# Kernel optimization log

Measured on AMD Instinct MI355X. Metric: run time of the kernel, lower is better.

Reference implementation:

```python
import jax, jax.numpy as jnp
import numpy as np

B, S, I, H, O = 256, 2048, 32, 128, 1


def setup_inputs() -> dict:
    key = jax.random.key(0)
    ks = jax.random.split(key, 9)
    sI = 1.0 / np.sqrt(I)
    sH = 1.0 / np.sqrt(H)
    sD = 1.0 / np.sqrt(H * S)
    return {
        "x": jax.random.normal(ks[0], (B, S, I), jnp.float32),
        "Wi": jax.random.normal(ks[1], (I, H), jnp.float32) * sI,
        "bi": jax.random.normal(ks[2], (H,), jnp.float32) * sI,
        "Wh": jax.random.normal(ks[3], (H, H), jnp.float32) * sH,
        "bh": jax.random.normal(ks[4], (H,), jnp.float32) * sH,
        "Wa": jax.random.normal(ks[5], (H, 1), jnp.float32) * sH,
        "ba": jax.random.normal(ks[6], (1,), jnp.float32) * sH,
        "Wd": jax.random.normal(ks[7], (H * S, O), jnp.float32) * sD,
        "bd": jax.random.normal(ks[8], (O,), jnp.float32) * sD,
        "resDepth": 4,
    }


def _branch_ids(seq_len: int, resDepth: int) -> np.ndarray:
    # Encodes the per-step branch of ResRNN_Cell.forward (static in i, resDepth):
    # 0: i==0 (set hstart, h0 stays zero)   1: i==lag-2 -> h0=tanh(hn+hstart)
    # 4: resDepth==1 -> h0=tanh(hn+h0)      2: i%resDepth==0 -> h0=tanh(hn+ht), ht=hn
    # 3: else -> h0=tanh(hn)
    br = np.full(seq_len, 3, dtype=np.int32)
    br[(np.arange(seq_len) % resDepth) == 0] = 2
    if resDepth == 1:
        br[:] = 4
    br[seq_len - 2] = 1
    br[0] = 0
    return br


def reference(x, Wi, bi, Wh, bh, Wa, ba, Wd, bd, resDepth):
    batch, seq_len, _ = x.shape
    hid = Wh.shape[0]
    br = _branch_ids(seq_len, int(resDepth))
    f0, f1, f2, f4 = (jnp.asarray(br == k) for k in (0, 1, 2, 4))
    xs = jnp.swapaxes(x, 0, 1)  # (S, B, I)
    z = jnp.zeros((batch, hid), x.dtype)

    def step(carry, inp):
        h0, ht, hstart = carry
        xt, g0, g1, g2, g4 = inp
        hn = xt @ Wi + bi + h0 @ Wh + bh  # (B, H)
        hstart = jnp.where(g0, hn, hstart)
        cand = jnp.where(g1, jnp.tanh(hn + hstart),
               jnp.where(g4, jnp.tanh(hn + h0),
               jnp.where(g2, jnp.tanh(hn + ht), jnp.tanh(hn))))
        h0n = jnp.where(g0, h0, cand)  # at i==0 h0 is NOT updated in the original
        htn = jnp.where(g2, hn, ht)
        return (h0n, htn, hstart), hn

    _, hiddens = jax.lax.scan(step, (z, z, z), (xs, f0, f1, f2, f4))
    # hiddens: (S, B, H) == torch.cat(outputs, 0)
    scores = hiddens @ Wa + ba  # (S, B, 1)
    # faithful to the original's .view((batchSize, -1)) on (S,B,1)-contiguous data
    att = jax.nn.softmax(scores.reshape(batch, seq_len), axis=-1)
    att = att.reshape(seq_len, batch, 1)
    weighted = hiddens * att  # (S, B, H)
    # faithful to .view(-1, hiddenNum * seq_len) on (S,B,H)-contiguous data
    flat = weighted.reshape(batch, seq_len * hid)
    return flat @ Wd + bd
```

## Files before the change

### kernel.cpp

```cpp
#include <hip/hip_runtime.h>
#include <math.h>

#define B_ 256
#define S_ 2048
#define I_ 32
#define H_ 128

typedef float v2f __attribute__((ext_vector_type(2)));
__device__ __forceinline__ v2f mk2(float a, float b) { v2f r; r.x = a; r.y = b; return r; }

__device__ __forceinline__ void pk_fma(v2f& d, v2f a, v2f b) {
    asm("v_pk_fma_f32 %0, %1, %2, %0" : "+v"(d) : "v"(a), "v"(b));
}
__device__ __forceinline__ void pk_fma_lo(v2f& d, v2f a, v2f b) {
    asm("v_pk_fma_f32 %0, %1, %2, %0 op_sel:[0,0,0] op_sel_hi:[0,1,1]"
        : "+v"(d) : "v"(a), "v"(b));
}
__device__ __forceinline__ void pk_fma_hi(v2f& d, v2f a, v2f b) {
    asm("v_pk_fma_f32 %0, %1, %2, %0 op_sel:[1,0,0] op_sel_hi:[1,1,1]"
        : "+v"(d) : "v"(a), "v"(b));
}

__device__ __forceinline__ void sync_lds() {
    asm volatile("" ::: "memory");
    asm volatile("s_waitcnt lgkmcnt(0)" ::: "memory");
    __builtin_amdgcn_s_barrier();
    asm volatile("" ::: "memory");
}

__device__ __forceinline__ float fast_tanh(float z) {
    float e = __expf(2.0f * z);
    return 1.0f - 2.0f / (e + 1.0f);
}

template <int CTRL>
__device__ __forceinline__ float dppf(float v) {
    return __int_as_float(__builtin_amdgcn_update_dpp(
        0, __float_as_int(v), CTRL, 0xF, 0xF, false));
}

__device__ __forceinline__ float swz_xor16(float v) {
    return __int_as_float(__builtin_amdgcn_ds_swizzle(__float_as_int(v), 0x401F));
}

#define PKQ(hv, q)                                                \
    pk_fma_lo(accA, mk2((hv).x, (hv).y), WhP[4 * (q) + 0]);       \
    pk_fma_hi(accA, mk2((hv).x, (hv).y), WhP[4 * (q) + 1]);       \
    pk_fma_lo(accB, mk2((hv).z, (hv).w), WhP[4 * (q) + 2]);       \
    pk_fma_hi(accB, mk2((hv).z, (hv).w), WhP[4 * (q) + 3]);

#define UP_REDUCE(RING)                                                       \
    {                                                                         \
      float r = uP;                                                           \
      r += dppf<0xB1>(r);                                                     \
      r += dppf<0x124>(r);                                                    \
      if ((l & 0xD) == 0)                                                     \
        ((float*)&pl_lds[RING][(w << 2) | ((l >> 4) & 3)])[(l >> 1) & 1] = r; \
    }

#define PL_COMBINE(RING, SIDX)                                                \
    {                                                                         \
      float2 pp = pl_lds[RING][l & 31];                                       \
      float px = pp.x, py = pp.y;                                             \
      px += dppf<0xB1>(px);  py += dppf<0xB1>(py);                            \
      px += dppf<0x4E>(px);  py += dppf<0x4E>(py);                            \
      px += dppf<0x141>(px); py += dppf<0x141>(py);                           \
      px += dppf<0x128>(px); py += dppf<0x128>(py);                           \
      px += swz_xor16(px);   py += swz_xor16(py);                             \
      if (l == 0) part[((SIDX) << 8) + b] = make_float2(px, py);              \
    }

#define MAT_CORE(XA, XB)                                                      \
    v2f xw01 = mk2(biasR, 0.0f);                                              \
    pk_fma(xw01, mk2((XA).x, (XA).y), WiP[0]);                                \
    pk_fma(xw01, mk2((XA).z, (XA).w), WiP[1]);                                \
    pk_fma(xw01, mk2((XB).x, (XB).y), WiP[2]);                                \
    pk_fma(xw01, mk2((XB).z, (XB).w), WiP[3]);                                \
    v2f accA = mk2(0.0f, 0.0f), accB = mk2(0.0f, 0.0f);                       \
    PKQ(hv0, 0) PKQ(hv1, 1) PKQ(hv2, 2) PKQ(hv3, 3)                           \
    float a0 = accA.x + accB.x;                                               \
    float a1 = accA.y + accB.y;                                               \
    a0 += dppf<0xB1>(a0);                                                     \
    a1 += dppf<0xB1>(a1);                                                     \
    float tt = kb0b ? a1 : a0;                                                \
    tt += xw01.x + xw01.y;                                                    \
    tt += dppf<0x4E>(tt);                                                     \
    tt += dppf<0x128>(tt);                                                    \
    const float hn = tt;

#define STEP_FULL(g, PH, XA, XB, CPH)                                         \
  {                                                                           \
    const int s_ = (g) * 8 + (PH);                                            \
    const float4* hsrc = (const float4*)&h0_lds[(PH) & 1][0];                 \
    float4 hv0 = hsrc[kg];                                                    \
    float4 hv1 = hsrc[kg + 8];                                                \
    float4 hv2 = hsrc[kg + 16];                                               \
    float4 hv3 = hsrc[kg + 24];                                               \
    if (s_ >= 1) UP_REDUCE(((PH) + 3) & 3)                                    \
    if (w == (PH) && s_ >= 2) PL_COMBINE(((PH) + 2) & 3, s_ - 2)              \
    MAT_CORE(XA, XB)                                                          \
    if (s_ < S_ - 2) {                                                        \
      const float4* xr = (const float4*)(xgrp + ((PH) + 2) * I_);             \
      (XA) = xr[0]; (XB) = xr[1];                                             \
    }                                                                         \
    uP = hn * (CPH);                                                          \
    float h0n;                                                                \
    if (s_ == 0)            { hstartR = hn; h0n = 0.0f; }                     \
    else if (s_ == S_ - 2)  { h0n = fast_tanh(hn + hstartR); }                \
    else if (rd == 1)       { h0n = fast_tanh(hn + h0R); }                    \
    else if (cnt == 0)      { h0n = fast_tanh(hn + htR); htR = hn; }          \
    else                    { h0n = fast_tanh(hn); }                          \
    h0R = h0n;                                                                \
    if (wmask) h0_lds[((PH) + 1) & 1][hf] = h0n;                              \
    cnt = (cnt + 1 == rd) ? 0 : cnt + 1;                                      \
    sync_lds();                                                               \
  }

#define STEP_LEAN4(g, PH, XA, XB, CPH)                                        \
  {                                                                           \
    const float4* hsrc = (const float4*)&h0_lds[(PH) & 1][0];                 \
    float4 hv0 = hsrc[kg];                                                    \
    float4 hv1 = hsrc[kg + 8];                                                \
    float4 hv2 = hsrc[kg + 16];                                               \
    float4 hv3 = hsrc[kg + 24];                                               \
    UP_REDUCE(((PH) + 3) & 3)                                                 \
    if (w == (PH)) PL_COMBINE(((PH) + 2) & 3, (g) * 8 + (PH) - 2)             \
    MAT_CORE(XA, XB)                                                          \
    {                                                                         \
      const float4* xr = (const float4*)(xgrp + ((PH) + 2) * I_);             \
      (XA) = xr[0]; (XB) = xr[1];                                             \
    }                                                                         \
    uP = hn * (CPH);                                                          \
    float h0n;                                                                \
    if (((PH) & 3) == 0) { h0n = fast_tanh(hn + htR); htR = hn; }             \
    else                 { h0n = fast_tanh(hn); }                             \
    if (wmask) h0_lds[((PH) + 1) & 1][hf] = h0n;                              \
    sync_lds();                                                               \
  }

#define STEP_LEAN(g, PH, XA, XB, CPH)                                         \
  {                                                                           \
    const float4* hsrc = (const float4*)&h0_lds[(PH) & 1][0];                 \
    float4 hv0 = hsrc[kg];                                                    \
    float4 hv1 = hsrc[kg + 8];                                                \
    float4 hv2 = hsrc[kg + 16];                                               \
    float4 hv3 = hsrc[kg + 24];                                               \
    UP_REDUCE(((PH) + 3) & 3)                                                 \
    if (w == (PH)) PL_COMBINE(((PH) + 2) & 3, (g) * 8 + (PH) - 2)             \
    MAT_CORE(XA, XB)                                                          \
    {                                                                         \
      const float4* xr = (const float4*)(xgrp + ((PH) + 2) * I_);             \
      (XA) = xr[0]; (XB) = xr[1];                                             \
    }                                                                         \
    uP = hn * (CPH);                                                          \
    const bool c0 = (cnt == 0);                                               \
    float resid = rd1 ? h0R : (c0 ? htR : 0.0f);                              \
    float h0n = fast_tanh(hn + resid);                                        \
    htR = (htup && c0) ? hn : htR;                                            \
    h0R = h0n;                                                                \
    if (wmask) h0_lds[((PH) + 1) & 1][hf] = h0n;                              \
    cnt = (cnt + 1 == rd) ? 0 : cnt + 1;                                      \
    sync_lds();                                                               \
  }

__global__ __launch_bounds__(512)
__attribute__((amdgpu_waves_per_eu(2, 2)))
void rnn_kernel(
    const float* __restrict__ x, const float* __restrict__ Wi,
    const float* __restrict__ bi, const float* __restrict__ Wh,
    const float* __restrict__ bh, const float* __restrict__ Wa,
    const float* __restrict__ Wd, const int* __restrict__ rdp,
    float2* __restrict__ part)
{
    const int b = blockIdx.x;
    const int t = threadIdx.x;
    const int w = t >> 6;
    const int l = t & 63;
    const int  kg    = (l & 3) | (((l >> 3) & 1) << 2);
    const int  hg    = ((l >> 2) & 1) | (((l >> 4) & 1) << 1)
                     | (((l >> 5) & 1) << 2);
    const int  hbase = 16 * w + 2 * hg;
    const int  hf    = hbase + (l & 1);
    const bool kb0b  = (l & 1);
    const bool wmask = ((l & 0xA) == 0);
    const int  i0x   = 8 * (((l >> 1) & 1) | (((l >> 3) & 1) << 1));

    __shared__ __align__(16) float h0_lds[2][H_];
    __shared__ __align__(8)  float2 pl_lds[4][32];

    const int rd = rdp[0];
    const bool rd1  = (rd == 1);
    const bool htup = !rd1;
    if (t < H_) h0_lds[0][t] = 0.0f;

    v2f WhP[16];
#pragma unroll
    for (int j = 0; j < 4; ++j)
#pragma unroll
        for (int c = 0; c < 4; ++c) {
            int k = 4 * kg + 32 * j + c;
            float2 wv = *(const float2*)(Wh + (size_t)k * H_ + hbase);
            WhP[4 * j + c] = mk2(wv.x, wv.y);
        }
    v2f WiP[4];
#pragma unroll
    for (int j = 0; j < 4; ++j) {
        float w0 = Wi[(size_t)(i0x + 2 * j) * H_ + hf];
        float w1 = Wi[(size_t)(i0x + 2 * j + 1) * H_ + hf];
        WiP[j] = mk2(w0, w1);
    }
    const float biasR = wmask ? (bi[hf] + bh[hf]) : 0.0f;

    const bool clsq = (l >> 1) & 1;
    const float waC = Wa[hf];
    float cph[8];
#pragma unroll
    for (int K = 0; K < 8; ++K)
        cph[K] = clsq ? Wd[(K << 15) + (b << 7) + hf] : waC;

    const float* xgrp = x + (size_t)b * (S_ * I_) + i0x;
    float4 xA0 = ((const float4*)xgrp)[0];
    float4 xB0 = ((const float4*)xgrp)[1];
    float4 xA1 = ((const float4*)(xgrp + I_))[0];
    float4 xB1 = ((const float4*)(xgrp + I_))[1];

    sync_lds();

    float htR = 0.f, hstartR = 0.f, h0R = 0.f;
    float uP = 0.f;
    int cnt = 0;

    {
        STEP_FULL(0, 0, xA0, xB0, cph[0])
        STEP_FULL(0, 1, xA1, xB1, cph[1])
        STEP_FULL(0, 2, xA0, xB0, cph[2])
        STEP_FULL(0, 3, xA1, xB1, cph[3])
        STEP_FULL(0, 4, xA0, xB0, cph[4])
        STEP_FULL(0, 5, xA1, xB1, cph[5])
        STEP_FULL(0, 6, xA0, xB0, cph[6])
        STEP_FULL(0, 7, xA1, xB1, cph[7])
        xgrp += 8 * I_;
    }
    if (rd == 4) {
        for (int g = 1; g < 255; ++g) {
            STEP_LEAN4(g, 0, xA0, xB0, cph[0])
            STEP_LEAN4(g, 1, xA1, xB1, cph[1])
            STEP_LEAN4(g, 2, xA0, xB0, cph[2])
            STEP_LEAN4(g, 3, xA1, xB1, cph[3])
            STEP_LEAN4(g, 4, xA0, xB0, cph[4])
            STEP_LEAN4(g, 5, xA1, xB1, cph[5])
            STEP_LEAN4(g, 6, xA0, xB0, cph[6])
            STEP_LEAN4(g, 7, xA1, xB1, cph[7])
            xgrp += 8 * I_;
        }
        cnt = 0;
    } else {
        for (int g = 1; g < 255; ++g) {
            STEP_LEAN(g, 0, xA0, xB0, cph[0])
            STEP_LEAN(g, 1, xA1, xB1, cph[1])
            STEP_LEAN(g, 2, xA0, xB0, cph[2])
            STEP_LEAN(g, 3, xA1, xB1, cph[3])
            STEP_LEAN(g, 4, xA0, xB0, cph[4])
            STEP_LEAN(g, 5, xA1, xB1, cph[5])
            STEP_LEAN(g, 6, xA0, xB0, cph[6])
            STEP_LEAN(g, 7, xA1, xB1, cph[7])
            xgrp += 8 * I_;
        }
    }
    {
        STEP_FULL(255, 0, xA0, xB0, cph[0])
        STEP_FULL(255, 1, xA1, xB1, cph[1])
        STEP_FULL(255, 2, xA0, xB0, cph[2])
        STEP_FULL(255, 3, xA1, xB1, cph[3])
        STEP_FULL(255, 4, xA0, xB0, cph[4])
        STEP_FULL(255, 5, xA1, xB1, cph[5])
        STEP_FULL(255, 6, xA0, xB0, cph[6])
        STEP_FULL(255, 7, xA1, xB1, cph[7])
    }

    UP_REDUCE(3)
    sync_lds();
    if (w == 0) PL_COMBINE(2, S_ - 2)
    if (w == 1) PL_COMBINE(3, S_ - 1)
}

__global__ __launch_bounds__(256) void attn_kernel(
    const float2* __restrict__ part, const float* __restrict__ bd,
    float* __restrict__ out)
{
    const int r = blockIdx.x;
    const int t = threadIdx.x;
    float sc[8], dv[8];
    float mx = -1e30f;
#pragma unroll
    for (int u = 0; u < 8; ++u) {
        int f = (r << 11) + (u << 8) + t;
        float2 a = part[f];
        sc[u] = a.x;
        dv[u] = a.y;
        mx = fmaxf(mx, sc[u]);
    }
    __shared__ float redm[4], redz[4], redw[4];
#pragma unroll
    for (int off = 32; off > 0; off >>= 1) mx = fmaxf(mx, __shfl_xor(mx, off, 64));
    if ((t & 63) == 0) redm[t >> 6] = mx;
    __syncthreads();
    mx = fmaxf(fmaxf(redm[0], redm[1]), fmaxf(redm[2], redm[3]));
    float z = 0.f, wv = 0.f;
#pragma unroll
    for (int u = 0; u < 8; ++u) {
        float e = __expf(sc[u] - mx);
        z += e;
        wv += e * dv[u];
    }
#pragma unroll
    for (int off = 32; off > 0; off >>= 1) {
        z += __shfl_xor(z, off, 64);
        wv += __shfl_xor(wv, off, 64);
    }
    if ((t & 63) == 0) { redz[t >> 6] = z; redw[t >> 6] = wv; }
    __syncthreads();
    if (t == 0) {
        float Z = redz[0] + redz[1] + redz[2] + redz[3];
        float W = redw[0] + redw[1] + redw[2] + redw[3];
        out[r] = bd[0] + W / Z;
    }
}

extern "C" void kernel_launch(void* const* d_in, const int* in_sizes, int n_in,
                              void* d_out, int out_size, void* d_ws, size_t ws_size,
                              hipStream_t stream) {
    const float* x  = (const float*)d_in[0];
    const float* Wi = (const float*)d_in[1];
    const float* bi = (const float*)d_in[2];
    const float* Wh = (const float*)d_in[3];
    const float* bh = (const float*)d_in[4];
    const float* Wa = (const float*)d_in[5];
    const float* Wd = (const float*)d_in[7];
    const float* bd = (const float*)d_in[8];
    const int*  rdp = (const int*)d_in[9];

    float2* part = (float2*)d_ws;

    rnn_kernel<<<B_, 512, 0, stream>>>(x, Wi, bi, Wh, bh, Wa, Wd, rdp, part);
    attn_kernel<<<B_, 256, 0, stream>>>(part, bd, (float*)d_out);
}
```

Measured before the change: 863.4 us.

## Remap recurrent matvec to 4 outputs x 8 k per lane with padded LDS

After: 863.1 us. About the same (-0.0%).

```diff
diff --git a/kernel.cpp b/kernel.cpp
--- a/kernel.cpp
+++ b/kernel.cpp
@@ -9,9 +9,6 @@
 typedef float v2f __attribute__((ext_vector_type(2)));
 __device__ __forceinline__ v2f mk2(float a, float b) { v2f r; r.x = a; r.y = b; return r; }
 
-__device__ __forceinline__ void pk_fma(v2f& d, v2f a, v2f b) {
-    asm("v_pk_fma_f32 %0, %1, %2, %0" : "+v"(d) : "v"(a), "v"(b));
-}
 __device__ __forceinline__ void pk_fma_lo(v2f& d, v2f a, v2f b) {
     asm("v_pk_fma_f32 %0, %1, %2, %0 op_sel:[0,0,0] op_sel_hi:[0,1,1]"
         : "+v"(d) : "v"(a), "v"(b));
@@ -43,19 +40,25 @@
     return __int_as_float(__builtin_amdgcn_ds_swizzle(__float_as_int(v), 0x401F));
 }
 
-#define PKQ(hv, q)                                                \
-    pk_fma_lo(accA, mk2((hv).x, (hv).y), WhP[4 * (q) + 0]);       \
-    pk_fma_hi(accA, mk2((hv).x, (hv).y), WhP[4 * (q) + 1]);       \
-    pk_fma_lo(accB, mk2((hv).z, (hv).w), WhP[4 * (q) + 2]);       \
-    pk_fma_hi(accB, mk2((hv).z, (hv).w), WhP[4 * (q) + 3]);
+#define CHP 12
+
+#define PKD(hv, base)                                             \
+    pk_fma_lo(acc01, mk2((hv).x, (hv).y), W01[(base) + 0]);       \
+    pk_fma_lo(acc23, mk2((hv).x, (hv).y), W23[(base) + 0]);       \
+    pk_fma_hi(acc01, mk2((hv).x, (hv).y), W01[(base) + 1]);       \
+    pk_fma_hi(acc23, mk2((hv).x, (hv).y), W23[(base) + 1]);       \
+    pk_fma_lo(acc01, mk2((hv).z, (hv).w), W01[(base) + 2]);       \
+    pk_fma_lo(acc23, mk2((hv).z, (hv).w), W23[(base) + 2]);       \
+    pk_fma_hi(acc01, mk2((hv).z, (hv).w), W01[(base) + 3]);       \
+    pk_fma_hi(acc23, mk2((hv).z, (hv).w), W23[(base) + 3]);
 
 #define UP_REDUCE(RING)                                                       \
     {                                                                         \
       float r = uP;                                                           \
       r += dppf<0xB1>(r);                                                     \
-      r += dppf<0x124>(r);                                                    \
-      if ((l & 0xD) == 0)                                                     \
-        ((float*)&pl_lds[RING][(w << 2) | ((l >> 4) & 3)])[(l >> 1) & 1] = r; \
+      r += dppf<0x4E>(r);                                                     \
+      if ((l & 0xB) == 0)                                                     \
+        ((float*)&pl_lds[RING][(w << 2) | ((l >> 4) & 3)])[(l >> 2) & 1] = r; \
     }
 
 #define PL_COMBINE(RING, SIDX)                                                \
@@ -70,38 +73,40 @@
       if (l == 0) part[((SIDX) << 8) + b] = make_float2(px, py);              \
     }
 
-#define MAT_CORE(XA, XB)                                                      \
-    v2f xw01 = mk2(biasR, 0.0f);                                              \
-    pk_fma(xw01, mk2((XA).x, (XA).y), WiP[0]);                                \
-    pk_fma(xw01, mk2((XA).z, (XA).w), WiP[1]);                                \
-    pk_fma(xw01, mk2((XB).x, (XB).y), WiP[2]);                                \
-    pk_fma(xw01, mk2((XB).z, (XB).w), WiP[3]);                                \
-    v2f accA = mk2(0.0f, 0.0f), accB = mk2(0.0f, 0.0f);                       \
-    PKQ(hv0, 0) PKQ(hv1, 1) PKQ(hv2, 2) PKQ(hv3, 3)                           \
-    float a0 = accA.x + accB.x;                                               \
-    float a1 = accA.y + accB.y;                                               \
-    a0 += dppf<0xB1>(a0);                                                     \
-    a1 += dppf<0xB1>(a1);                                                     \
-    float tt = kb0b ? a1 : a0;                                                \
-    tt += xw01.x + xw01.y;                                                    \
-    tt += dppf<0x4E>(tt);                                                     \
+#define MAT_CORE(XS)                                                          \
+    v2f acc01 = bias01, acc23 = bias23;                                       \
+    pk_fma_lo(acc01, mk2((XS).x, (XS).y), WiF01[0]);                          \
+    pk_fma_hi(acc01, mk2((XS).x, (XS).y), WiF01[1]);                          \
+    pk_fma_lo(acc23, mk2((XS).x, (XS).y), WiF23[0]);                          \
+    pk_fma_hi(acc23, mk2((XS).x, (XS).y), WiF23[1]);                          \
+    PKD(hvA, 0) PKD(hvB, 4)                                                   \
+    float p0 = acc01.x + dppf<0x141>(acc01.x);                                \
+    float p1 = acc01.y + dppf<0x141>(acc01.y);                                \
+    float p2 = acc23.x + dppf<0x141>(acc23.x);                                \
+    float p3 = acc23.y + dppf<0x141>(acc23.y);                                \
+    float s01x = p0 + dppf<0xB1>(p0);                                         \
+    float s01y = p1 + dppf<0xB1>(p1);                                         \
+    float s23x = p2 + dppf<0xB1>(p2);                                         \
+    float s23y = p3 + dppf<0xB1>(p3);                                         \
+    float t0 = kb0 ? s01y : s01x;                                             \
+    float t1 = kb0 ? s23y : s23x;                                             \
+    t0 += dppf<0x4E>(t0);                                                     \
+    t1 += dppf<0x4E>(t1);                                                     \
+    float tt = kb1 ? t1 : t0;                                                 \
     tt += dppf<0x128>(tt);                                                    \
     const float hn = tt;
 
-#define STEP_FULL(g, PH, XA, XB, CPH)                                         \
+#define STEP_FULL(g, PH, XS, CPH)                                             \
   {                                                                           \
     const int s_ = (g) * 8 + (PH);                                            \
-    const float4* hsrc = (const float4*)&h0_lds[(PH) & 1][0];                 \
-    float4 hv0 = hsrc[kg];                                                    \
-    float4 hv1 = hsrc[kg + 8];                                                \
-    float4 hv2 = hsrc[kg + 16];                                               \
-    float4 hv3 = hsrc[kg + 24];                                               \
+    const float* hb = &h0_lds[(PH) & 1][0];                                   \
+    float4 hvA = *(const float4*)(hb + rdoff);                                \
+    float4 hvB = *(const float4*)(hb + rdoff + 4);                            \
     if (s_ >= 1) UP_REDUCE(((PH) + 3) & 3)                                    \
     if (w == (PH) && s_ >= 2) PL_COMBINE(((PH) + 2) & 3, s_ - 2)              \
-    MAT_CORE(XA, XB)                                                          \
+    MAT_CORE(XS)                                                              \
     if (s_ < S_ - 2) {                                                        \
-      const float4* xr = (const float4*)(xgrp + ((PH) + 2) * I_);             \
-      (XA) = xr[0]; (XB) = xr[1];                                             \
+      (XS) = *(const float2*)(xgrp + ((PH) + 2) * I_);                        \
     }                                                                         \
     uP = hn * (CPH);                                                          \
     float h0n;                                                                \
@@ -111,54 +116,44 @@
     else if (cnt == 0)      { h0n = fast_tanh(hn + htR); htR = hn; }          \
     else                    { h0n = fast_tanh(hn); }                          \
     h0R = h0n;                                                                \
-    if (wmask) h0_lds[((PH) + 1) & 1][hf] = h0n;                              \
+    if (wmask) h0_lds[((PH) + 1) & 1][hwoff] = h0n;                           \
     cnt = (cnt + 1 == rd) ? 0 : cnt + 1;                                      \
     sync_lds();                                                               \
   }
 
-#define STEP_LEAN4(g, PH, XA, XB, CPH)                                        \
+#define STEP_LEAN4(g, PH, XS, CPH)                                            \
   {                                                                           \
-    const float4* hsrc = (const float4*)&h0_lds[(PH) & 1][0];                 \
-    float4 hv0 = hsrc[kg];                                                    \
-    float4 hv1 = hsrc[kg + 8];                                                \
-    float4 hv2 = hsrc[kg + 16];                                               \
-    float4 hv3 = hsrc[kg + 24];                                               \
+    const float* hb = &h0_lds[(PH) & 1][0];                                   \
+    float4 hvA = *(const float4*)(hb + rdoff);                                \
+    float4 hvB = *(const float4*)(hb + rdoff + 4);                            \
     UP_REDUCE(((PH) + 3) & 3)                                                 \
     if (w == (PH)) PL_COMBINE(((PH) + 2) & 3, (g) * 8 + (PH) - 2)             \
-    MAT_CORE(XA, XB)                                                          \
-    {                                                                         \
-      const float4* xr = (const float4*)(xgrp + ((PH) + 2) * I_);             \
-      (XA) = xr[0]; (XB) = xr[1];                                             \
-    }                                                                         \
+    MAT_CORE(XS)                                                              \
+    (XS) = *(const float2*)(xgrp + ((PH) + 2) * I_);                          \
     uP = hn * (CPH);                                                          \
     float h0n;                                                                \
     if (((PH) & 3) == 0) { h0n = fast_tanh(hn + htR); htR = hn; }             \
     else                 { h0n = fast_tanh(hn); }                             \
-    if (wmask) h0_lds[((PH) + 1) & 1][hf] = h0n;                              \
+    if (wmask) h0_lds[((PH) + 1) & 1][hwoff] = h0n;                           \
     sync_lds();                                                               \
   }
 
-#define STEP_LEAN(g, PH, XA, XB, CPH)                                         \
+#define STEP_LEAN(g, PH, XS, CPH)                                             \
   {                                                                           \
-    const float4* hsrc = (const float4*)&h0_lds[(PH) & 1][0];                 \
-    float4 hv0 = hsrc[kg];                                                    \
-    float4 hv1 = hsrc[kg + 8];                                                \
-    float4 hv2 = hsrc[kg + 16];                                               \
-    float4 hv3 = hsrc[kg + 24];                                               \
+    const float* hb = &h0_lds[(PH) & 1][0];                                   \
+    float4 hvA = *(const float4*)(hb + rdoff);                                \
+    float4 hvB = *(const float4*)(hb + rdoff + 4);                            \
     UP_REDUCE(((PH) + 3) & 3)                                                 \
     if (w == (PH)) PL_COMBINE(((PH) + 2) & 3, (g) * 8 + (PH) - 2)             \
-    MAT_CORE(XA, XB)                                                          \
-    {                                                                         \
-      const float4* xr = (const float4*)(xgrp + ((PH) + 2) * I_);             \
-      (XA) = xr[0]; (XB) = xr[1];                                             \
-    }                                                                         \
+    MAT_CORE(XS)                                                              \
+    (XS) = *(const float2*)(xgrp + ((PH) + 2) * I_);                          \
     uP = hn * (CPH);                                                          \
     const bool c0 = (cnt == 0);                                               \
     float resid = rd1 ? h0R : (c0 ? htR : 0.0f);                              \
     float h0n = fast_tanh(hn + resid);                                        \
     htR = (htup && c0) ? hn : htR;                                            \
     h0R = h0n;                                                                \
-    if (wmask) h0_lds[((PH) + 1) & 1][hf] = h0n;                              \
+    if (wmask) h0_lds[((PH) + 1) & 1][hwoff] = h0n;                           \
     cnt = (cnt + 1 == rd) ? 0 : cnt + 1;                                      \
     sync_lds();                                                               \
   }
@@ -176,53 +171,57 @@
     const int t = threadIdx.x;
     const int w = t >> 6;
     const int l = t & 63;
-    const int  kg    = (l & 3) | (((l >> 3) & 1) << 2);
-    const int  hg    = ((l >> 2) & 1) | (((l >> 4) & 1) << 1)
-                     | (((l >> 5) & 1) << 2);
-    const int  hbase = 16 * w + 2 * hg;
-    const int  hf    = hbase + (l & 1);
-    const bool kb0b  = (l & 1);
-    const bool wmask = ((l & 0xA) == 0);
-    const int  i0x   = 8 * (((l >> 1) & 1) | (((l >> 3) & 1) << 1));
-
-    __shared__ __align__(16) float h0_lds[2][H_];
+    const int  kg4   = l & 15;
+    const int  hg2   = (l >> 4) & 3;
+    const int  hbase = 16 * w + 4 * hg2;
+    const int  hf    = hbase + (l & 3);
+    const bool kb0   = (l & 1);
+    const bool kb1   = (l >> 1) & 1;
+    const bool wmask = ((l & 0xC) == 0);
+    const int  rdoff = kg4 * CHP;
+    const int  hwoff = (hf >> 3) * CHP + (hf & 7);
+
+    __shared__ __align__(16) float h0_lds[2][16 * CHP];
     __shared__ __align__(8)  float2 pl_lds[4][32];
 
     const int rd = rdp[0];
     const bool rd1  = (rd == 1);
     const bool htup = !rd1;
-    if (t < H_) h0_lds[0][t] = 0.0f;
-
-    v2f WhP[16];
-#pragma unroll
-    for (int j = 0; j < 4; ++j)
-#pragma unroll
-        for (int c = 0; c < 4; ++c) {
-            int k = 4 * kg + 32 * j + c;
-            float2 wv = *(const float2*)(Wh + (size_t)k * H_ + hbase);
-            WhP[4 * j + c] = mk2(wv.x, wv.y);
-        }
-    v2f WiP[4];
-#pragma unroll
-    for (int j = 0; j < 4; ++j) {
-        float w0 = Wi[(size_t)(i0x + 2 * j) * H_ + hf];
-        float w1 = Wi[(size_t)(i0x + 2 * j + 1) * H_ + hf];
-        WiP[j] = mk2(w0, w1);
-    }
-    const float biasR = wmask ? (bi[hf] + bh[hf]) : 0.0f;
-
-    const bool clsq = (l >> 1) & 1;
+    if (t < 16 * CHP) h0_lds[0][t] = 0.0f;
+
+    v2f W01[8], W23[8];
+#pragma unroll
+    for (int c = 0; c < 8; ++c) {
+        int k = 8 * kg4 + c;
+        float4 q = *(const float4*)(Wh + (size_t)k * H_ + hbase);
+        W01[c] = mk2(q.x, q.y);
+        W23[c] = mk2(q.z, q.w);
+    }
+    const int i0 = 2 * kg4;
+    v2f WiF01[2], WiF23[2];
+#pragma unroll
+    for (int j = 0; j < 2; ++j) {
+        float2 a = *(const float2*)(Wi + (size_t)(i0 + j) * H_ + hbase);
+        float2 c = *(const float2*)(Wi + (size_t)(i0 + j) * H_ + hbase + 2);
+        WiF01[j] = mk2(a.x, a.y);
+        WiF23[j] = mk2(c.x, c.y);
+    }
+    const bool k0g = (kg4 == 0);
+    const v2f bias01 = k0g ? mk2(bi[hbase] + bh[hbase],
+                                 bi[hbase + 1] + bh[hbase + 1]) : mk2(0.f, 0.f);
+    const v2f bias23 = k0g ? mk2(bi[hbase + 2] + bh[hbase + 2],
+                                 bi[hbase + 3] + bh[hbase + 3]) : mk2(0.f, 0.f);
+
+    const bool clsq = (l >> 2) & 1;
     const float waC = Wa[hf];
     float cph[8];
 #pragma unroll
     for (int K = 0; K < 8; ++K)
         cph[K] = clsq ? Wd[(K << 15) + (b << 7) + hf] : waC;
 
-    const float* xgrp = x + (size_t)b * (S_ * I_) + i0x;
-    float4 xA0 = ((const float4*)xgrp)[0];
-    float4 xB0 = ((const float4*)xgrp)[1];
-    float4 xA1 = ((const float4*)(xgrp + I_))[0];
-    float4 xB1 = ((const float4*)(xgrp + I_))[1];
+    const float* xgrp = x + (size_t)b * (S_ * I_) + i0;
+    float2 xS0 = *(const float2*)xgrp;
+    float2 xS1 = *(const float2*)(xgrp + I_);
 
     sync_lds();
 
@@ -231,51 +230,51 @@
     int cnt = 0;
 
     {
-        STEP_FULL(0, 0, xA0, xB0, cph[0])
-        STEP_FULL(0, 1, xA1, xB1, cph[1])
-        STEP_FULL(0, 2, xA0, xB0, cph[2])
-        STEP_FULL(0, 3, xA1, xB1, cph[3])
-        STEP_FULL(0, 4, xA0, xB0, cph[4])
-        STEP_FULL(0, 5, xA1, xB1, cph[5])
-        STEP_FULL(0, 6, xA0, xB0, cph[6])
-        STEP_FULL(0, 7, xA1, xB1, cph[7])
+        STEP_FULL(0, 0, xS0, cph[0])
+        STEP_FULL(0, 1, xS1, cph[1])
+        STEP_FULL(0, 2, xS0, cph[2])
+        STEP_FULL(0, 3, xS1, cph[3])
+        STEP_FULL(0, 4, xS0, cph[4])
+        STEP_FULL(0, 5, xS1, cph[5])
+        STEP_FULL(0, 6, xS0, cph[6])
+        STEP_FULL(0, 7, xS1, cph[7])
         xgrp += 8 * I_;
     }
     if (rd == 4) {
         for (int g = 1; g < 255; ++g) {
-            STEP_LEAN4(g, 0, xA0, xB0, cph[0])
-            STEP_LEAN4(g, 1, xA1, xB1, cph[1])
-            STEP_LEAN4(g, 2, xA0, xB0, cph[2])
-            STEP_LEAN4(g, 3, xA1, xB1, cph[3])
-            STEP_LEAN4(g, 4, xA0, xB0, cph[4])
-            STEP_LEAN4(g, 5, xA1, xB1, cph[5])
-            STEP_LEAN4(g, 6, xA0, xB0, cph[6])
-            STEP_LEAN4(g, 7, xA1, xB1, cph[7])
+            STEP_LEAN4(g, 0, xS0, cph[0])
+            STEP_LEAN4(g, 1, xS1, cph[1])
+            STEP_LEAN4(g, 2, xS0, cph[2])
+            STEP_LEAN4(g, 3, xS1, cph[3])
+            STEP_LEAN4(g, 4, xS0, cph[4])
+            STEP_LEAN4(g, 5, xS1, cph[5])
+            STEP_LEAN4(g, 6, xS0, cph[6])
+            STEP_LEAN4(g, 7, xS1, cph[7])
             xgrp += 8 * I_;
         }
         cnt = 0;
     } else {
         for (int g = 1; g < 255; ++g) {
-            STEP_LEAN(g, 0, xA0, xB0, cph[0])
-            STEP_LEAN(g, 1, xA1, xB1, cph[1])
-            STEP_LEAN(g, 2, xA0, xB0, cph[2])
-            STEP_LEAN(g, 3, xA1, xB1, cph[3])
-            STEP_LEAN(g, 4, xA0, xB0, cph[4])
-            STEP_LEAN(g, 5, xA1, xB1, cph[5])
-            STEP_LEAN(g, 6, xA0, xB0, cph[6])
-            STEP_LEAN(g, 7, xA1, xB1, cph[7])
+            STEP_LEAN(g, 0, xS0, cph[0])
+            STEP_LEAN(g, 1, xS1, cph[1])
+            STEP_LEAN(g, 2, xS0, cph[2])
+            STEP_LEAN(g, 3, xS1, cph[3])
+            STEP_LEAN(g, 4, xS0, cph[4])
+            STEP_LEAN(g, 5, xS1, cph[5])
+            STEP_LEAN(g, 6, xS0, cph[6])
+            STEP_LEAN(g, 7, xS1, cph[7])
             xgrp += 8 * I_;
         }
     }
     {
-        STEP_FULL(255, 0, xA0, xB0, cph[0])
-        STEP_FULL(255, 1, xA1, xB1, cph[1])
-        STEP_FULL(255, 2, xA0, xB0, cph[2])
-        STEP_FULL(255, 3, xA1, xB1, cph[3])
-        STEP_FULL(255, 4, xA0, xB0, cph[4])
-        STEP_FULL(255, 5, xA1, xB1, cph[5])
-        STEP_FULL(255, 6, xA0, xB0, cph[6])
-        STEP_FULL(255, 7, xA1, xB1, cph[7])
+        STEP_FULL(255, 0, xS0, cph[0])
+        STEP_FULL(255, 1, xS1, cph[1])
+        STEP_FULL(255, 2, xS0, cph[2])
+        STEP_FULL(255, 3, xS1, cph[3])
+        STEP_FULL(255, 4, xS0, cph[4])
+        STEP_FULL(255, 5, xS1, cph[5])
+        STEP_FULL(255, 6, xS0, cph[6])
+        STEP_FULL(255, 7, xS1, cph[7])
     }
 
     UP_REDUCE(3)
```
